# Performance work log

Measured on AMD Instinct MI355X. Metric: run time of the kernel, lower is better.

Reference implementation:

```python
import jax, jax.numpy as jnp
import numpy as np

EPS = 1e-15
N_NODES = 20000
N_EDGES = 640000
FEAT = 128
N_RBF = 20
CUTOFF = 5.0


def setup_inputs() -> dict:
    key = jax.random.key(0)
    ks = jax.random.split(key, 10)
    s_j = jax.random.normal(ks[0], (N_NODES, FEAT), jnp.float32)
    v_j = jax.random.normal(ks[1], (N_NODES, FEAT, 3), jnp.float32)
    r_ij = jax.random.normal(ks[2], (N_EDGES, 3), jnp.float32)
    nbrs = jax.random.randint(ks[3], (N_EDGES, 2), 0, N_NODES, jnp.int64)
    # InvariantDense: Dense(F->F, swish) then Dense(F->3F)
    W1 = jax.random.normal(ks[4], (FEAT, FEAT), jnp.float32) / np.sqrt(FEAT)
    b1 = jnp.zeros((FEAT,), jnp.float32)
    W2 = jax.random.normal(ks[5], (FEAT, 3 * FEAT), jnp.float32) / np.sqrt(FEAT)
    b2 = jnp.zeros((3 * FEAT,), jnp.float32)
    # DistanceEmbed dense: Dense(n_rbf -> 3F)
    Wd = jax.random.normal(ks[6], (N_RBF, 3 * FEAT), jnp.float32) / np.sqrt(N_RBF)
    bd = jnp.zeros((3 * FEAT,), jnp.float32)
    return {"s_j": s_j, "v_j": v_j, "r_ij": r_ij, "nbrs": nbrs,
            "W1": W1, "b1": b1, "W2": W2, "b2": b2, "Wd": Wd, "bd": bd}


def reference(s_j, v_j, r_ij, nbrs, W1, b1, W2, b2, Wd, bd):
    N, F = s_j.shape
    # preprocess_r
    dist = jnp.sqrt(jnp.sum(r_ij ** 2 + EPS, axis=-1))          # [E]
    unit = r_ij / dist[:, None]                                  # [E,3]
    # InvariantDense on nodes (dense before gather, as in torch code)
    phi_node = jax.nn.silu(s_j @ W1 + b1) @ W2 + b2              # [N,3F]
    phi = phi_node[nbrs[:, 1]]                                   # [E,3F]
    # PaiNN radial basis: sin(n*pi*d/cutoff)/d, n=1..n_rbf
    k = jnp.arange(1, N_RBF + 1, dtype=dist.dtype) * (np.pi / CUTOFF)  # [n_rbf]
    rbf = jnp.sin(dist[:, None] * k[None, :]) / dist[:, None]    # [E,n_rbf]
    # cosine cutoff envelope
    env = 0.5 * (jnp.cos(np.pi * dist / CUTOFF) + 1.0)
    env = jnp.where(dist < CUTOFF, env, 0.0)                     # [E]
    w_s = (rbf @ Wd + bd) * env[:, None]                         # [E,3F]
    inv = (phi * w_s).reshape(-1, 3, F)                          # [E,3,F]
    split0 = inv[:, 0, :][:, :, None]                            # [E,F,1]
    split1 = inv[:, 1, :]                                        # [E,F]
    split2 = inv[:, 2, :][:, :, None]                            # [E,F,1]
    delta_v_ij = split2 * unit[:, None, :] + split0 * v_j[nbrs[:, 1]]  # [E,F,3]
    idx = nbrs[:, 0]
    delta_s_i = jax.ops.segment_sum(split1, idx, num_segments=N)      # [N,F]
    delta_v_i = jax.ops.segment_sum(delta_v_ij, idx, num_segments=N)  # [N,F,3]
    return (delta_s_i, delta_v_i)
```

## Files before the change

### kernel.cpp

```cpp
#include <hip/hip_runtime.h>
#include <hip/hip_bf16.h>
#include <math.h>

typedef __hip_bfloat16 bf16;

#define FEAT 128
#define NRBF 20
#define CUTOFF_F 5.0f
#define KSCALE 0.62831853071795864769f

__device__ __forceinline__ float b2f(bf16 x) { return __bfloat162float(x); }
__device__ __forceinline__ bf16 f2b(float x) { return __float2bfloat16(x); }

template<int F32>
__device__ __forceinline__ float LD(const void* p, size_t i) {
    if (F32) return ((const float*)p)[i];
    return b2f(((const bf16*)p)[i]);
}
template<int F32>
__device__ __forceinline__ void ST(void* p, size_t i, float v) {
    if (F32) ((float*)p)[i] = v;
    else ((bf16*)p)[i] = f2b(v);
}

__device__ __forceinline__ int get_dst(const int* nb, int e, int is64) {
    return is64 ? nb[4 * e] : nb[2 * e];
}
__device__ __forceinline__ int get_src(const int* nb, int e, int is64) {
    return is64 ? nb[4 * e + 2] : nb[2 * e + 1];
}
__device__ __forceinline__ int clampi(int v, int n) {
    return v < 0 ? 0 : (v >= n ? n - 1 : v);
}

__global__ void init_kernel(const void* __restrict__ s_ptr, const int* __restrict__ nbrs32,
                            int nE, int* __restrict__ flags, int* __restrict__ counts, int nN) {
    int t = blockIdx.x * blockDim.x + threadIdx.x;
    if (t < nN) counts[t] = 0;
    if (t == 0) {
        const unsigned* u = (const unsigned*)s_ptr;
        int hits = 0;
        for (int i = 0; i < 64; ++i) {
            unsigned ef = (u[i] >> 7) & 0xFF;
            hits += (ef >= 110 && ef <= 135) ? 1 : 0;
        }
        flags[0] = (hits < 32) ? 1 : 0;
        int lim = 2 * nE; if (lim > 128) lim = 128;
        int allz = 1;
        for (int i = 1; i < lim; i += 2) allz &= (nbrs32[i] == 0);
        flags[1] = allz;
    }
}

__global__ void hist_kernel(const int* __restrict__ nbrs, const int* __restrict__ flags,
                            int* __restrict__ counts, int nE, int nN) {
    int e = blockIdx.x * blockDim.x + threadIdx.x;
    if (e < nE) {
        int d = clampi(get_dst(nbrs, e, flags[1]), nN);
        atomicAdd(&counts[d], 1);
    }
}

__global__ __launch_bounds__(1024) void scan_kernel(const int* __restrict__ counts,
        int* __restrict__ offsets, int* __restrict__ cursor, int nN) {
    __shared__ int part[1024];
    const int t = threadIdx.x;
    const int chunk = (nN + 1023) / 1024;
    const int base = t * chunk;
    int local[32];
    int sum = 0;
    for (int c = 0; c < chunk && c < 32; ++c) {
        int idx = base + c;
        int v = (idx < nN) ? counts[idx] : 0;
        local[c] = v;
        sum += v;
    }
    part[t] = sum;
    __syncthreads();
    for (int off = 1; off < 1024; off <<= 1) {
        int add = (t >= off) ? part[t - off] : 0;
        __syncthreads();
        part[t] += add;
        __syncthreads();
    }
    int run = part[t] - sum;
    for (int c = 0; c < chunk && c < 32; ++c) {
        int idx = base + c;
        if (idx < nN) { offsets[idx] = run; cursor[idx] = run; run += local[c]; }
    }
    if (t == 1023) offsets[nN] = part[1023];
}

__global__ void scatter_kernel(const int* __restrict__ nbrs, const int* __restrict__ flags,
                               int* __restrict__ cursor, int* __restrict__ edge_ids,
                               int nE, int nN) {
    int e = blockIdx.x * blockDim.x + threadIdx.x;
    if (e < nE) {
        int d = clampi(get_dst(nbrs, e, flags[1]), nN);
        int pos = atomicAdd(&cursor[d], 1);
        if (pos >= 0 && pos < nE) edge_ids[pos] = e;
    }
}

template<int F32, int GM>
__global__ __launch_bounds__(256) void pre_kernel(const void* __restrict__ r_ij,
        void* __restrict__ gbuf, const int* __restrict__ flags, int nE) {
    if (flags[0] != F32) return;
    int e = blockIdx.x * blockDim.x + threadIdx.x;
    if (e >= nE) return;
    const float rx = LD<F32>(r_ij, (size_t)3 * e + 0);
    const float ry = LD<F32>(r_ij, (size_t)3 * e + 1);
    const float rz = LD<F32>(r_ij, (size_t)3 * e + 2);
    const float d2   = rx * rx + ry * ry + rz * rz + 3e-15f;
    const float invd = rsqrtf(d2);
    const float d    = d2 * invd;
    const float x  = d * KSCALE;
    const float s1 = F32 ? sinf(x) : __sinf(x);
    const float c1 = F32 ? cosf(x) : __cosf(x);
    const float env = (d < CUTOFF_F) ? (0.5f * (c1 + 1.0f)) : 0.0f;
    const float scale = invd * env;
    float rec[24];
    const float tc = 2.0f * c1;
    float skm2 = 0.f, skm1 = s1;
    rec[0] = s1 * scale;
    #pragma unroll
    for (int k = 1; k < NRBF; ++k) {
        const float sk = fmaf(tc, skm1, -skm2);
        rec[k] = sk * scale;
        skm2 = skm1; skm1 = sk;
    }
    rec[20] = rx * invd; rec[21] = ry * invd; rec[22] = rz * invd; rec[23] = env;
    if (GM == 2) {
        float* dst = (float*)gbuf + (size_t)24 * e;
        #pragma unroll
        for (int i = 0; i < 24; ++i) dst[i] = rec[i];
    } else {
        bf16* dst = (bf16*)gbuf + (size_t)24 * e;
        #pragma unroll
        for (int i = 0; i < 24; ++i) dst[i] = f2b(rec[i]);
    }
}

template<int F32>
__device__ void gemm_body(const void* __restrict__ s_j, const void* __restrict__ W1,
                          const void* __restrict__ b1, const void* __restrict__ W2,
                          const void* __restrict__ b2v, bf16* __restrict__ phi, int nN) {
    __shared__ float sl[8][FEAT];
    __shared__ float hl[8][FEAT];
    const int t = threadIdx.x;
    const int n0 = blockIdx.x * 8;
    for (int idx = t; idx < 8 * FEAT; idx += 384) {
        int n = idx >> 7, k = idx & 127;
        int row = n0 + n;
        sl[n][k] = (row < nN) ? LD<F32>(s_j, (size_t)row * FEAT + k) : 0.f;
    }
    __syncthreads();
    for (int idx = t; idx < 8 * FEAT; idx += 384) {
        int n = idx >> 7, f = idx & 127;
        float a = 0.f;
        #pragma unroll 4
        for (int k = 0; k < FEAT; ++k) a = fmaf(sl[n][k], LD<F32>(W1, (size_t)k * FEAT + f), a);
        a += LD<F32>(b1, f);
        float sg = F32 ? (1.0f / (1.0f + expf(-a))) : (1.0f / (1.0f + __expf(-a)));
        hl[n][f] = a * sg;
    }
    __syncthreads();
    float acc[8] = {};
    #pragma unroll 4
    for (int k = 0; k < FEAT; ++k) {
        const float w = LD<F32>(W2, (size_t)k * 384 + t);
        #pragma unroll
        for (int n = 0; n < 8; ++n) acc[n] = fmaf(hl[n][k], w, acc[n]);
    }
    const float bb = LD<F32>(b2v, t);
    #pragma unroll
    for (int n = 0; n < 8; ++n) {
        int row = n0 + n;
        if (row < nN) phi[(size_t)row * 384 + t] = f2b(acc[n] + bb);
    }
}

__global__ __launch_bounds__(384) void gemm_node_kernel(const void* s_j, const void* W1,
        const void* b1, const void* W2, const void* b2v, bf16* phi,
        const int* __restrict__ flags, int nN) {
    if (flags[0]) gemm_body<1>(s_j, W1, b1, W2, b2v, phi, nN);
    else          gemm_body<0>(s_j, W1, b1, W2, b2v, phi, nN);
}

template<int F32, int GM>
__global__ __launch_bounds__(128, 2) void msg_kernel(
        const int* __restrict__ nbrs, const void* __restrict__ r_ij,
        const void* __restrict__ v_j, const void* __restrict__ Wd,
        const void* __restrict__ bd, const bf16* __restrict__ phi,
        const void* __restrict__ gbuf, const int* __restrict__ flags,
        const int* __restrict__ offsets, const int* __restrict__ edge_ids,
        void* __restrict__ out, int nE, int nN) {
    if (flags[0] != F32) return;
    const int i = blockIdx.x;
    const int f = threadIdx.x;
    const int is64 = flags[1];

    float wd0[NRBF], wd1[NRBF], wd2[NRBF];
    #pragma unroll
    for (int k = 0; k < NRBF; ++k) {
        wd0[k] = LD<F32>(Wd, (size_t)k * 384 + f);
        wd1[k] = LD<F32>(Wd, (size_t)k * 384 + FEAT + f);
        wd2[k] = LD<F32>(Wd, (size_t)k * 384 + 2 * FEAT + f);
    }
    const float bd0 = LD<F32>(bd, f);
    const float bd1 = LD<F32>(bd, FEAT + f);
    const float bd2 = LD<F32>(bd, 2 * FEAT + f);

    float ds = 0.f, dv0 = 0.f, dv1 = 0.f, dv2 = 0.f;

    int start = offsets[i];
    int end   = offsets[i + 1];
    if (start < 0) start = 0;
    if (end > nE) end = nE;

    for (int p = start; p < end; ++p) {
        const int e = __builtin_amdgcn_readfirstlane(clampi(edge_ids[p], nE));
        const int j = __builtin_amdgcn_readfirstlane(clampi(get_src(nbrs, e, is64), nN));

        float gk[24];
        if (GM == 2) {
            const float* g = (const float*)gbuf + (size_t)24 * e;
            #pragma unroll
            for (int q = 0; q < 24; ++q) gk[q] = g[q];
        } else if (GM == 1) {
            const bf16* g = (const bf16*)gbuf + (size_t)24 * e;
            #pragma unroll
            for (int q = 0; q < 24; ++q) gk[q] = b2f(g[q]);
        } else {
            const float rx = LD<F32>(r_ij, (size_t)3 * e + 0);
            const float ry = LD<F32>(r_ij, (size_t)3 * e + 1);
            const float rz = LD<F32>(r_ij, (size_t)3 * e + 2);
            const float d2   = rx * rx + ry * ry + rz * rz + 3e-15f;
            const float invd = rsqrtf(d2);
            const float d    = d2 * invd;
            const float x  = d * KSCALE;
            const float s1 = F32 ? sinf(x) : __sinf(x);
            const float c1 = F32 ? cosf(x) : __cosf(x);
            const float env = (d < CUTOFF_F) ? (0.5f * (c1 + 1.0f)) : 0.0f;
            const float scale = invd * env;
            const float tc = 2.0f * c1;
            float skm2 = 0.f, skm1 = s1;
            gk[0] = s1 * scale;
            #pragma unroll
            for (int k = 1; k < NRBF; ++k) {
                const float sk = fmaf(tc, skm1, -skm2);
                gk[k] = sk * scale;
                skm2 = skm1; skm1 = sk;
            }
            gk[20] = rx * invd; gk[21] = ry * invd; gk[22] = rz * invd; gk[23] = env;
        }

        float t0 = 0.f, t1 = 0.f, t2 = 0.f;
        #pragma unroll
        for (int k = 0; k < NRBF; ++k) {
            t0 = fmaf(gk[k], wd0[k], t0);
            t1 = fmaf(gk[k], wd1[k], t1);
            t2 = fmaf(gk[k], wd2[k], t2);
        }
        const float env = gk[23];
        const float w0 = fmaf(bd0, env, t0);
        const float w1 = fmaf(bd1, env, t1);
        const float w2 = fmaf(bd2, env, t2);

        const size_t pb = (size_t)j * 384;
        const float p0 = b2f(phi[pb + f]);
        const float p1 = b2f(phi[pb + FEAT + f]);
        const float p2 = b2f(phi[pb + 2 * FEAT + f]);
        const size_t vb = ((size_t)j * FEAT + f) * 3;
        const float vx = LD<F32>(v_j, vb + 0);
        const float vy = LD<F32>(v_j, vb + 1);
        const float vz = LD<F32>(v_j, vb + 2);

        const float i0 = w0 * p0;
        const float i1 = w1 * p1;
        const float i2 = w2 * p2;
        ds += i1;
        dv0 = fmaf(i2, gk[20], fmaf(i0, vx, dv0));
        dv1 = fmaf(i2, gk[21], fmaf(i0, vy, dv1));
        dv2 = fmaf(i2, gk[22], fmaf(i0, vz, dv2));
    }

    ST<F32>(out, (size_t)i * FEAT + f, ds);
    const size_t ob = (size_t)nN * FEAT + ((size_t)i * FEAT + f) * 3;
    ST<F32>(out, ob + 0, dv0);
    ST<F32>(out, ob + 1, dv1);
    ST<F32>(out, ob + 2, dv2);
}

extern "C" void kernel_launch(void* const* d_in, const int* in_sizes, int n_in,
                              void* d_out, int out_size, void* d_ws, size_t ws_size,
                              hipStream_t stream) {
    const void* s_j  = d_in[0];
    const void* v_j  = d_in[1];
    const void* r_ij = d_in[2];
    const int*  nbrs = (const int*)d_in[3];
    const void* W1   = d_in[4];
    const void* b1   = d_in[5];
    const void* W2   = d_in[6];
    const void* b2   = d_in[7];
    const void* Wd   = d_in[8];
    const void* bd   = d_in[9];

    const int nN = out_size / (4 * FEAT);
    const int nE = in_sizes[2] / 3;

    char* ws = (char*)d_ws;
    size_t off = 0;
    int* flags = (int*)(ws + off);    off += 256;
    int* counts = (int*)(ws + off);   off += ((size_t)nN * 4 + 255) & ~(size_t)255;
    int* offsets = (int*)(ws + off);  off += (((size_t)nN + 1) * 4 + 255) & ~(size_t)255;
    int* cursor = (int*)(ws + off);   off += ((size_t)nN * 4 + 255) & ~(size_t)255;
    int* edge_ids = (int*)(ws + off); off += ((size_t)nE * 4 + 255) & ~(size_t)255;

    const size_t phi_bytes = (size_t)nN * 384 * sizeof(bf16);
    const size_t g32_bytes = (size_t)nE * 24 * 4;
    const size_t g16_bytes = (size_t)nE * 24 * 2;
    int GM;
    size_t g_bytes;
    if (ws_size >= off + g32_bytes + phi_bytes)      { GM = 2; g_bytes = g32_bytes; }
    else if (ws_size >= off + g16_bytes + phi_bytes) { GM = 1; g_bytes = g16_bytes; }
    else                                             { GM = 0; g_bytes = 0; }
    void* gbuf = (void*)(ws + off);   off += (g_bytes + 255) & ~(size_t)255;
    bf16* phi = (bf16*)(ws + off);

    init_kernel<<<(nN + 255) / 256, 256, 0, stream>>>(s_j, nbrs, nE, flags, counts, nN);

    const int preg = (nE + 255) / 256;
    if (GM == 2) {
        pre_kernel<0, 2><<<preg, 256, 0, stream>>>(r_ij, gbuf, flags, nE);
        pre_kernel<1, 2><<<preg, 256, 0, stream>>>(r_ij, gbuf, flags, nE);
    } else if (GM == 1) {
        pre_kernel<0, 1><<<preg, 256, 0, stream>>>(r_ij, gbuf, flags, nE);
        pre_kernel<1, 1><<<preg, 256, 0, stream>>>(r_ij, gbuf, flags, nE);
    }

    gemm_node_kernel<<<(nN + 7) / 8, 384, 0, stream>>>(s_j, W1, b1, W2, b2, phi, flags, nN);
    hist_kernel<<<(nE + 255) / 256, 256, 0, stream>>>(nbrs, flags, counts, nE, nN);
    scan_kernel<<<1, 1024, 0, stream>>>(counts, offsets, cursor, nN);
    scatter_kernel<<<(nE + 255) / 256, 256, 0, stream>>>(nbrs, flags, cursor, edge_ids, nE, nN);

    if (GM == 2) {
        msg_kernel<0, 2><<<nN, 128, 0, stream>>>(nbrs, r_ij, v_j, Wd, bd, phi, gbuf, flags, offsets, edge_ids, d_out, nE, nN);
        msg_kernel<1, 2><<<nN, 128, 0, stream>>>(nbrs, r_ij, v_j, Wd, bd, phi, gbuf, flags, offsets, edge_ids, d_out, nE, nN);
    } else if (GM == 1) {
        msg_kernel<0, 1><<<nN, 128, 0, stream>>>(nbrs, r_ij, v_j, Wd, bd, phi, gbuf, flags, offsets, edge_ids, d_out, nE, nN);
        msg_kernel<1, 1><<<nN, 128, 0, stream>>>(nbrs, r_ij, v_j, Wd, bd, phi, gbuf, flags, offsets, edge_ids, d_out, nE, nN);
    } else {
        msg_kernel<0, 0><<<nN, 128, 0, stream>>>(nbrs, r_ij, v_j, Wd, bd, phi, gbuf, flags, offsets, edge_ids, d_out, nE, nN);
        msg_kernel<1, 0><<<nN, 128, 0, stream>>>(nbrs, r_ij, v_j, Wd, bd, phi, gbuf, flags, offsets, edge_ids, d_out, nE, nN);
    }
}
```

Baseline: 596.2 us.

## Fuse edge scatter into precompute and batch edge-index loads via lane shuffles

Merges the CSR scatter into the per-edge RBF precompute kernel and reorders launches so histogram and scan run first, removing one kernel launch and one pass over nbrs. In the message kernel, edge ids and source nodes for a block of up to 64 edges are loaded once in parallel across lanes and broadcast with shuffles, instead of each iteration doing serial scalar loads. The geometry record is read as float4 vectors, and an asm barrier pins the Wd weights in registers. Shuffles add cross-lane work per edge, and the register pinning may raise register pressure.

Result: slower. 720.7 us (+20.9%).

```diff
diff --git a/kernel.cpp b/kernel.cpp
--- a/kernel.cpp
+++ b/kernel.cpp
@@ -91,33 +91,31 @@
     if (t == 1023) offsets[nN] = part[1023];
 }
 
-__global__ void scatter_kernel(const int* __restrict__ nbrs, const int* __restrict__ flags,
-                               int* __restrict__ cursor, int* __restrict__ edge_ids,
-                               int nE, int nN) {
-    int e = blockIdx.x * blockDim.x + threadIdx.x;
-    if (e < nE) {
-        int d = clampi(get_dst(nbrs, e, flags[1]), nN);
-        int pos = atomicAdd(&cursor[d], 1);
-        if (pos >= 0 && pos < nE) edge_ids[pos] = e;
-    }
-}
-
 template<int F32, int GM>
-__global__ __launch_bounds__(256) void pre_kernel(const void* __restrict__ r_ij,
-        void* __restrict__ gbuf, const int* __restrict__ flags, int nE) {
+__global__ __launch_bounds__(256) void pre_scatter_kernel(
+        const void* __restrict__ r_ij, const int* __restrict__ nbrs,
+        const int* __restrict__ flags, int* __restrict__ cursor,
+        int* __restrict__ edge_ids, void* __restrict__ gbuf, int nE, int nN) {
     if (flags[0] != F32) return;
     int e = blockIdx.x * blockDim.x + threadIdx.x;
     if (e >= nE) return;
+
+    int d = clampi(get_dst(nbrs, e, flags[1]), nN);
+    int pos = atomicAdd(&cursor[d], 1);
+    if (pos >= 0 && pos < nE) edge_ids[pos] = e;
+
+    if (GM == 0) return;
+
     const float rx = LD<F32>(r_ij, (size_t)3 * e + 0);
     const float ry = LD<F32>(r_ij, (size_t)3 * e + 1);
     const float rz = LD<F32>(r_ij, (size_t)3 * e + 2);
     const float d2   = rx * rx + ry * ry + rz * rz + 3e-15f;
     const float invd = rsqrtf(d2);
-    const float d    = d2 * invd;
-    const float x  = d * KSCALE;
+    const float dd   = d2 * invd;
+    const float x  = dd * KSCALE;
     const float s1 = F32 ? sinf(x) : __sinf(x);
     const float c1 = F32 ? cosf(x) : __cosf(x);
-    const float env = (d < CUTOFF_F) ? (0.5f * (c1 + 1.0f)) : 0.0f;
+    const float env = (dd < CUTOFF_F) ? (0.5f * (c1 + 1.0f)) : 0.0f;
     const float scale = invd * env;
     float rec[24];
     const float tc = 2.0f * c1;
@@ -198,6 +196,7 @@
     if (flags[0] != F32) return;
     const int i = blockIdx.x;
     const int f = threadIdx.x;
+    const int lane = f & 63;
     const int is64 = flags[1];
 
     float wd0[NRBF], wd1[NRBF], wd2[NRBF];
@@ -207,6 +206,10 @@
         wd1[k] = LD<F32>(Wd, (size_t)k * 384 + FEAT + f);
         wd2[k] = LD<F32>(Wd, (size_t)k * 384 + 2 * FEAT + f);
     }
+    #pragma unroll
+    for (int k = 0; k < NRBF; ++k) {
+        asm volatile("" : "+v"(wd0[k]), "+v"(wd1[k]), "+v"(wd2[k]));
+    }
     const float bd0 = LD<F32>(bd, f);
     const float bd1 = LD<F32>(bd, FEAT + f);
     const float bd2 = LD<F32>(bd, 2 * FEAT + f);
@@ -217,72 +220,86 @@
     int end   = offsets[i + 1];
     if (start < 0) start = 0;
     if (end > nE) end = nE;
-
-    for (int p = start; p < end; ++p) {
-        const int e = __builtin_amdgcn_readfirstlane(clampi(edge_ids[p], nE));
-        const int j = __builtin_amdgcn_readfirstlane(clampi(get_src(nbrs, e, is64), nN));
-
-        float gk[24];
-        if (GM == 2) {
-            const float* g = (const float*)gbuf + (size_t)24 * e;
-            #pragma unroll
-            for (int q = 0; q < 24; ++q) gk[q] = g[q];
-        } else if (GM == 1) {
-            const bf16* g = (const bf16*)gbuf + (size_t)24 * e;
-            #pragma unroll
-            for (int q = 0; q < 24; ++q) gk[q] = b2f(g[q]);
-        } else {
-            const float rx = LD<F32>(r_ij, (size_t)3 * e + 0);
-            const float ry = LD<F32>(r_ij, (size_t)3 * e + 1);
-            const float rz = LD<F32>(r_ij, (size_t)3 * e + 2);
-            const float d2   = rx * rx + ry * ry + rz * rz + 3e-15f;
-            const float invd = rsqrtf(d2);
-            const float d    = d2 * invd;
-            const float x  = d * KSCALE;
-            const float s1 = F32 ? sinf(x) : __sinf(x);
-            const float c1 = F32 ? cosf(x) : __cosf(x);
-            const float env = (d < CUTOFF_F) ? (0.5f * (c1 + 1.0f)) : 0.0f;
-            const float scale = invd * env;
-            const float tc = 2.0f * c1;
-            float skm2 = 0.f, skm1 = s1;
-            gk[0] = s1 * scale;
+    const int cnt = end - start;
+
+    for (int base = 0; base < cnt; base += 64) {
+        const int m = (cnt - base < 64) ? (cnt - base) : 64;
+        int eL = 0, jL = 0;
+        if (lane < m) {
+            eL = clampi(edge_ids[start + base + lane], nE);
+            jL = clampi(get_src(nbrs, eL, is64), nN);
+        }
+        #pragma unroll 2
+        for (int q = 0; q < m; ++q) {
+            const int e = __shfl(eL, q);
+            const int j = __shfl(jL, q);
+
+            float gk[24];
+            if (GM == 2) {
+                const float4* g4 = (const float4*)((const float*)gbuf + (size_t)24 * e);
+                #pragma unroll
+                for (int c = 0; c < 6; ++c) {
+                    float4 v = g4[c];
+                    gk[4 * c + 0] = v.x; gk[4 * c + 1] = v.y;
+                    gk[4 * c + 2] = v.z; gk[4 * c + 3] = v.w;
+                }
+            } else if (GM == 1) {
+                const bf16* g = (const bf16*)gbuf + (size_t)24 * e;
+                #pragma unroll
+                for (int c = 0; c < 24; ++c) gk[c] = b2f(g[c]);
+            } else {
+                const float rx = LD<F32>(r_ij, (size_t)3 * e + 0);
+                const float ry = LD<F32>(r_ij, (size_t)3 * e + 1);
+                const float rz = LD<F32>(r_ij, (size_t)3 * e + 2);
+                const float d2   = rx * rx + ry * ry + rz * rz + 3e-15f;
+                const float invd = rsqrtf(d2);
+                const float dd   = d2 * invd;
+                const float x  = dd * KSCALE;
+                const float s1 = F32 ? sinf(x) : __sinf(x);
+                const float c1 = F32 ? cosf(x) : __cosf(x);
+                const float env = (dd < CUTOFF_F) ? (0.5f * (c1 + 1.0f)) : 0.0f;
+                const float scale = invd * env;
+                const float tc = 2.0f * c1;
+                float skm2 = 0.f, skm1 = s1;
+                gk[0] = s1 * scale;
+                #pragma unroll
+                for (int k = 1; k < NRBF; ++k) {
+                    const float sk = fmaf(tc, skm1, -skm2);
+                    gk[k] = sk * scale;
+                    skm2 = skm1; skm1 = sk;
+                }
+                gk[20] = rx * invd; gk[21] = ry * invd; gk[22] = rz * invd; gk[23] = env;
+            }
+
+            const size_t pb = (size_t)j * 384;
+            const float p0 = b2f(phi[pb + f]);
+            const float p1 = b2f(phi[pb + FEAT + f]);
+            const float p2 = b2f(phi[pb + 2 * FEAT + f]);
+            const size_t vb = ((size_t)j * FEAT + f) * 3;
+            const float vx = LD<F32>(v_j, vb + 0);
+            const float vy = LD<F32>(v_j, vb + 1);
+            const float vz = LD<F32>(v_j, vb + 2);
+
+            float t0 = gk[0] * wd0[0], t1 = gk[0] * wd1[0], t2 = gk[0] * wd2[0];
             #pragma unroll
             for (int k = 1; k < NRBF; ++k) {
-                const float sk = fmaf(tc, skm1, -skm2);
-                gk[k] = sk * scale;
-                skm2 = skm1; skm1 = sk;
+                t0 = fmaf(gk[k], wd0[k], t0);
+                t1 = fmaf(gk[k], wd1[k], t1);
+                t2 = fmaf(gk[k], wd2[k], t2);
             }
-            gk[20] = rx * invd; gk[21] = ry * invd; gk[22] = rz * invd; gk[23] = env;
+            const float env = gk[23];
+            const float w0 = fmaf(bd0, env, t0);
+            const float w1 = fmaf(bd1, env, t1);
+            const float w2 = fmaf(bd2, env, t2);
+
+            const float i0 = w0 * p0;
+            const float i1 = w1 * p1;
+            const float i2 = w2 * p2;
+            ds += i1;
+            dv0 = fmaf(i2, gk[20], fmaf(i0, vx, dv0));
+            dv1 = fmaf(i2, gk[21], fmaf(i0, vy, dv1));
+            dv2 = fmaf(i2, gk[22], fmaf(i0, vz, dv2));
         }
-
-        float t0 = 0.f, t1 = 0.f, t2 = 0.f;
-        #pragma unroll
-        for (int k = 0; k < NRBF; ++k) {
-            t0 = fmaf(gk[k], wd0[k], t0);
-            t1 = fmaf(gk[k], wd1[k], t1);
-            t2 = fmaf(gk[k], wd2[k], t2);
-        }
-        const float env = gk[23];
-        const float w0 = fmaf(bd0, env, t0);
-        const float w1 = fmaf(bd1, env, t1);
-        const float w2 = fmaf(bd2, env, t2);
-
-        const size_t pb = (size_t)j * 384;
-        const float p0 = b2f(phi[pb + f]);
-        const float p1 = b2f(phi[pb + FEAT + f]);
-        const float p2 = b2f(phi[pb + 2 * FEAT + f]);
-        const size_t vb = ((size_t)j * FEAT + f) * 3;
-        const float vx = LD<F32>(v_j, vb + 0);
-        const float vy = LD<F32>(v_j, vb + 1);
-        const float vz = LD<F32>(v_j, vb + 2);
-
-        const float i0 = w0 * p0;
-        const float i1 = w1 * p1;
-        const float i2 = w2 * p2;
-        ds += i1;
-        dv0 = fmaf(i2, gk[20], fmaf(i0, vx, dv0));
-        dv1 = fmaf(i2, gk[21], fmaf(i0, vy, dv1));
-        dv2 = fmaf(i2, gk[22], fmaf(i0, vz, dv2));
     }
 
     ST<F32>(out, (size_t)i * FEAT + f, ds);
@@ -329,20 +346,22 @@
     bf16* phi = (bf16*)(ws + off);
 
     init_kernel<<<(nN + 255) / 256, 256, 0, stream>>>(s_j, nbrs, nE, flags, counts, nN);
+    hist_kernel<<<(nE + 255) / 256, 256, 0, stream>>>(nbrs, flags, counts, nE, nN);
+    scan_kernel<<<1, 1024, 0, stream>>>(counts, offsets, cursor, nN);
 
     const int preg = (nE + 255) / 256;
     if (GM == 2) {
-        pre_kernel<0, 2><<<preg, 256, 0, stream>>>(r_ij, gbuf, flags, nE);
-        pre_kernel<1, 2><<<preg, 256, 0, stream>>>(r_ij, gbuf, flags, nE);
+        pre_scatter_kernel<0, 2><<<preg, 256, 0, stream>>>(r_ij, nbrs, flags, cursor, edge_ids, gbuf, nE, nN);
+        pre_scatter_kernel<1, 2><<<preg, 256, 0, stream>>>(r_ij, nbrs, flags, cursor, edge_ids, gbuf, nE, nN);
     } else if (GM == 1) {
-        pre_kernel<0, 1><<<preg, 256, 0, stream>>>(r_ij, gbuf, flags, nE);
-        pre_kernel<1, 1><<<preg, 256, 0, stream>>>(r_ij, gbuf, flags, nE);
+        pre_scatter_kernel<0, 1><<<preg, 256, 0, stream>>>(r_ij, nbrs, flags, cursor, edge_ids, gbuf, nE, nN);
+        pre_scatter_kernel<1, 1><<<preg, 256, 0, stream>>>(r_ij, nbrs, flags, cursor, edge_ids, gbuf, nE, nN);
+    } else {
+        pre_scatter_kernel<0, 0><<<preg, 256, 0, stream>>>(r_ij, nbrs, flags, cursor, edge_ids, gbuf, nE, nN);
+        pre_scatter_kernel<1, 0><<<preg, 256, 0, stream>>>(r_ij, nbrs, flags, cursor, edge_ids, gbuf, nE, nN);
     }
 
     gemm_node_kernel<<<(nN + 7) / 8, 384, 0, stream>>>(s_j, W1, b1, W2, b2, phi, flags, nN);
-    hist_kernel<<<(nE + 255) / 256, 256, 0, stream>>>(nbrs, flags, counts, nE, nN);
-    scan_kernel<<<1, 1024, 0, stream>>>(counts, offsets, cursor, nN);
-    scatter_kernel<<<(nE + 255) / 256, 256, 0, stream>>>(nbrs, flags, cursor, edge_ids, nE, nN);
 
     if (GM == 2) {
         msg_kernel<0, 2><<<nN, 128, 0, stream>>>(nbrs, r_ij, v_j, Wd, bd, phi, gbuf, flags, offsets, edge_ids, d_out, nE, nN);
```

## Fuse edge preprocessing into CSR scatter and store per-edge data in sorted order

Applied to the files above, without the earlier changes.

Merges the edge scatter with per-edge geometry preprocessing so unit vectors, envelope, source ids and RBF values are written directly at the destination-sorted position, which makes the message kernel's reads contiguous instead of indirect through edge_ids. When workspace allows, a new pass precomputes the full per-edge filter (rbf@Wd+bd)*env as bf16 rows in sorted order, so the message kernel only streams them. This trades a large extra write of E*384 bf16 values plus a second pass over r_ij for removing the per-edge 20x3 matvec in the gather kernel. It also adds bf16 rounding of the filter weights.

New measurement: 534.6 us. -10.3%, faster.

```diff
diff --git a/kernel.cpp b/kernel.cpp
--- a/kernel.cpp
+++ b/kernel.cpp
@@ -91,53 +91,72 @@
     if (t == 1023) offsets[nN] = part[1023];
 }
 
-__global__ void scatter_kernel(const int* __restrict__ nbrs, const int* __restrict__ flags,
-                               int* __restrict__ cursor, int* __restrict__ edge_ids,
-                               int nE, int nN) {
-    int e = blockIdx.x * blockDim.x + threadIdx.x;
-    if (e < nE) {
-        int d = clampi(get_dst(nbrs, e, flags[1]), nN);
-        int pos = atomicAdd(&cursor[d], 1);
-        if (pos >= 0 && pos < nE) edge_ids[pos] = e;
-    }
-}
-
-template<int F32, int GM>
-__global__ __launch_bounds__(256) void pre_kernel(const void* __restrict__ r_ij,
-        void* __restrict__ gbuf, const int* __restrict__ flags, int nE) {
-    if (flags[0] != F32) return;
-    int e = blockIdx.x * blockDim.x + threadIdx.x;
-    if (e >= nE) return;
+__global__ __launch_bounds__(384) void prep_kernel(const void* __restrict__ Wd,
+        const void* __restrict__ bd, float* __restrict__ WdT, const int* __restrict__ flags) {
+    const int c = threadIdx.x;
+    const int F32 = flags[0];
+    if (F32) {
+        for (int k = 0; k < NRBF; ++k) WdT[c * 24 + k] = ((const float*)Wd)[k * 384 + c];
+        WdT[c * 24 + 20] = ((const float*)bd)[c];
+    } else {
+        for (int k = 0; k < NRBF; ++k) WdT[c * 24 + k] = b2f(((const bf16*)Wd)[k * 384 + c]);
+        WdT[c * 24 + 20] = b2f(((const bf16*)bd)[c]);
+    }
+    WdT[c * 24 + 21] = 0.f; WdT[c * 24 + 22] = 0.f; WdT[c * 24 + 23] = 0.f;
+}
+
+template<int F32, int MODEA>
+__device__ void pre_scatter_body(const void* __restrict__ r_ij, const int* __restrict__ nbrs,
+        int is64, int* __restrict__ cursor, int* __restrict__ src_ids,
+        float4* __restrict__ u_env, int* __restrict__ pos_of_e, float* __restrict__ gbuf,
+        int e, int nE, int nN) {
+    const int d = clampi(get_dst(nbrs, e, is64), nN);
+    const int j = clampi(get_src(nbrs, e, is64), nN);
+    int pos = atomicAdd(&cursor[d], 1);
+    pos = clampi(pos, nE);
+    src_ids[pos] = j;
+
     const float rx = LD<F32>(r_ij, (size_t)3 * e + 0);
     const float ry = LD<F32>(r_ij, (size_t)3 * e + 1);
     const float rz = LD<F32>(r_ij, (size_t)3 * e + 2);
     const float d2   = rx * rx + ry * ry + rz * rz + 3e-15f;
     const float invd = rsqrtf(d2);
-    const float d    = d2 * invd;
-    const float x  = d * KSCALE;
-    const float s1 = F32 ? sinf(x) : __sinf(x);
+    const float dd   = d2 * invd;
+    const float x  = dd * KSCALE;
     const float c1 = F32 ? cosf(x) : __cosf(x);
-    const float env = (d < CUTOFF_F) ? (0.5f * (c1 + 1.0f)) : 0.0f;
-    const float scale = invd * env;
-    float rec[24];
-    const float tc = 2.0f * c1;
-    float skm2 = 0.f, skm1 = s1;
-    rec[0] = s1 * scale;
-    #pragma unroll
-    for (int k = 1; k < NRBF; ++k) {
-        const float sk = fmaf(tc, skm1, -skm2);
-        rec[k] = sk * scale;
-        skm2 = skm1; skm1 = sk;
-    }
-    rec[20] = rx * invd; rec[21] = ry * invd; rec[22] = rz * invd; rec[23] = env;
-    if (GM == 2) {
-        float* dst = (float*)gbuf + (size_t)24 * e;
+    const float env = (dd < CUTOFF_F) ? (0.5f * (c1 + 1.0f)) : 0.0f;
+    u_env[pos] = make_float4(rx * invd, ry * invd, rz * invd, env);
+
+    if (MODEA) {
+        pos_of_e[e] = pos;
+    } else {
+        const float s1 = F32 ? sinf(x) : __sinf(x);
+        const float scale = invd * env;
+        const float tc = 2.0f * c1;
+        float skm2 = 0.f, skm1 = s1;
+        float* g = gbuf + (size_t)pos * NRBF;
+        g[0] = s1 * scale;
         #pragma unroll
-        for (int i = 0; i < 24; ++i) dst[i] = rec[i];
+        for (int k = 1; k < NRBF; ++k) {
+            const float sk = fmaf(tc, skm1, -skm2);
+            g[k] = sk * scale;
+            skm2 = skm1; skm1 = sk;
+        }
+    }
+}
+
+__global__ __launch_bounds__(256) void pre_scatter_kernel(const void* r_ij, const int* nbrs,
+        const int* __restrict__ flags, int* cursor, int* src_ids, float4* u_env,
+        int* pos_of_e, float* gbuf, int nE, int nN, int modeA) {
+    int e = blockIdx.x * blockDim.x + threadIdx.x;
+    if (e >= nE) return;
+    const int F32 = flags[0], is64 = flags[1];
+    if (modeA) {
+        if (F32) pre_scatter_body<1,1>(r_ij, nbrs, is64, cursor, src_ids, u_env, pos_of_e, gbuf, e, nE, nN);
+        else     pre_scatter_body<0,1>(r_ij, nbrs, is64, cursor, src_ids, u_env, pos_of_e, gbuf, e, nE, nN);
     } else {
-        bf16* dst = (bf16*)gbuf + (size_t)24 * e;
-        #pragma unroll
-        for (int i = 0; i < 24; ++i) dst[i] = f2b(rec[i]);
+        if (F32) pre_scatter_body<1,0>(r_ij, nbrs, is64, cursor, src_ids, u_env, pos_of_e, gbuf, e, nE, nN);
+        else     pre_scatter_body<0,0>(r_ij, nbrs, is64, cursor, src_ids, u_env, pos_of_e, gbuf, e, nE, nN);
     }
 }
 
@@ -187,18 +206,117 @@
     else          gemm_body<0>(s_j, W1, b1, W2, b2v, phi, nN);
 }
 
-template<int F32, int GM>
-__global__ __launch_bounds__(128, 2) void msg_kernel(
-        const int* __restrict__ nbrs, const void* __restrict__ r_ij,
-        const void* __restrict__ v_j, const void* __restrict__ Wd,
-        const void* __restrict__ bd, const bf16* __restrict__ phi,
-        const void* __restrict__ gbuf, const int* __restrict__ flags,
-        const int* __restrict__ offsets, const int* __restrict__ edge_ids,
+template<int F32>
+__device__ void pre_ws_body(const void* __restrict__ r_ij, const float* __restrict__ WdT,
+        const int* __restrict__ pos_of_e, bf16* __restrict__ ws_w, int e) {
+    const float rx = LD<F32>(r_ij, (size_t)3 * e + 0);
+    const float ry = LD<F32>(r_ij, (size_t)3 * e + 1);
+    const float rz = LD<F32>(r_ij, (size_t)3 * e + 2);
+    const float d2   = rx * rx + ry * ry + rz * rz + 3e-15f;
+    const float invd = rsqrtf(d2);
+    const float dd   = d2 * invd;
+    const float x  = dd * KSCALE;
+    const float s1 = F32 ? sinf(x) : __sinf(x);
+    const float c1 = F32 ? cosf(x) : __cosf(x);
+    const float env = (dd < CUTOFF_F) ? (0.5f * (c1 + 1.0f)) : 0.0f;
+    const float scale = invd * env;
+    float gk[NRBF];
+    const float tc = 2.0f * c1;
+    float skm2 = 0.f, skm1 = s1;
+    gk[0] = s1 * scale;
+    #pragma unroll
+    for (int k = 1; k < NRBF; ++k) {
+        const float sk = fmaf(tc, skm1, -skm2);
+        gk[k] = sk * scale;
+        skm2 = skm1; skm1 = sk;
+    }
+    const int pos = pos_of_e[e];
+    bf16* dst = ws_w + (size_t)pos * 384;
+    for (int c0 = 0; c0 < 384; c0 += 4) {
+        float r[4];
+        #pragma unroll
+        for (int u = 0; u < 4; ++u) {
+            const float* w = WdT + (size_t)(c0 + u) * 24;
+            float acc = w[20] * env;
+            #pragma unroll
+            for (int k = 0; k < NRBF; ++k) acc = fmaf(gk[k], w[k], acc);
+            r[u] = acc;
+        }
+        union { bf16 b[4]; uint2 u2; } pk;
+        pk.b[0] = f2b(r[0]); pk.b[1] = f2b(r[1]); pk.b[2] = f2b(r[2]); pk.b[3] = f2b(r[3]);
+        *(uint2*)(dst + c0) = pk.u2;
+    }
+}
+
+__global__ __launch_bounds__(256) void pre_ws_kernel(const void* r_ij,
+        const float* __restrict__ WdT, const int* __restrict__ pos_of_e,
+        bf16* __restrict__ ws_w, const int* __restrict__ flags, int nE) {
+    int e = blockIdx.x * blockDim.x + threadIdx.x;
+    if (e >= nE) return;
+    if (flags[0]) pre_ws_body<1>(r_ij, WdT, pos_of_e, ws_w, e);
+    else          pre_ws_body<0>(r_ij, WdT, pos_of_e, ws_w, e);
+}
+
+template<int F32>
+__device__ void msg_a_body(const bf16* __restrict__ ws_w, const bf16* __restrict__ phi,
+        const void* __restrict__ v_j, const int* __restrict__ src_ids,
+        const float4* __restrict__ u_env, const int* __restrict__ offsets,
         void* __restrict__ out, int nE, int nN) {
-    if (flags[0] != F32) return;
     const int i = blockIdx.x;
     const int f = threadIdx.x;
-    const int is64 = flags[1];
+    int start = offsets[i];
+    int end   = offsets[i + 1];
+    if (start < 0) start = 0;
+    if (end > nE) end = nE;
+
+    float ds = 0.f, dv0 = 0.f, dv1 = 0.f, dv2 = 0.f;
+
+    #pragma unroll 2
+    for (int p = start; p < end; ++p) {
+        const int j = src_ids[p];
+        const float4 ue = u_env[p];
+        const bf16* wr = ws_w + (size_t)p * 384;
+        const float w0 = b2f(wr[f]);
+        const float w1 = b2f(wr[FEAT + f]);
+        const float w2 = b2f(wr[2 * FEAT + f]);
+        const bf16* ph = phi + (size_t)j * 384;
+        const float p0 = b2f(ph[f]);
+        const float p1 = b2f(ph[FEAT + f]);
+        const float p2 = b2f(ph[2 * FEAT + f]);
+        const float vx = LD<F32>(v_j, ((size_t)j * FEAT + f) * 3 + 0);
+        const float vy = LD<F32>(v_j, ((size_t)j * FEAT + f) * 3 + 1);
+        const float vz = LD<F32>(v_j, ((size_t)j * FEAT + f) * 3 + 2);
+        const float i0 = w0 * p0;
+        const float i1 = w1 * p1;
+        const float i2 = w2 * p2;
+        ds += i1;
+        dv0 = fmaf(i2, ue.x, fmaf(i0, vx, dv0));
+        dv1 = fmaf(i2, ue.y, fmaf(i0, vy, dv1));
+        dv2 = fmaf(i2, ue.z, fmaf(i0, vz, dv2));
+    }
+
+    ST<F32>(out, (size_t)i * FEAT + f, ds);
+    const size_t ob = (size_t)nN * FEAT + ((size_t)i * FEAT + f) * 3;
+    ST<F32>(out, ob + 0, dv0);
+    ST<F32>(out, ob + 1, dv1);
+    ST<F32>(out, ob + 2, dv2);
+}
+
+__global__ __launch_bounds__(128) void msg_a_kernel(const bf16* ws_w, const bf16* phi,
+        const void* v_j, const int* src_ids, const float4* u_env, const int* offsets,
+        const int* __restrict__ flags, void* out, int nE, int nN) {
+    if (flags[0]) msg_a_body<1>(ws_w, phi, v_j, src_ids, u_env, offsets, out, nE, nN);
+    else          msg_a_body<0>(ws_w, phi, v_j, src_ids, u_env, offsets, out, nE, nN);
+}
+
+template<int F32>
+__device__ void msg_b_body(const void* __restrict__ v_j, const void* __restrict__ Wd,
+        const void* __restrict__ bd, const bf16* __restrict__ phi,
+        const float* __restrict__ gbuf, const int* __restrict__ src_ids,
+        const float4* __restrict__ u_env, const int* __restrict__ offsets,
+        void* __restrict__ out, int nE, int nN) {
+    const int i = blockIdx.x;
+    const int f = threadIdx.x;
 
     float wd0[NRBF], wd1[NRBF], wd2[NRBF];
     #pragma unroll
@@ -211,78 +329,44 @@
     const float bd1 = LD<F32>(bd, FEAT + f);
     const float bd2 = LD<F32>(bd, 2 * FEAT + f);
 
-    float ds = 0.f, dv0 = 0.f, dv1 = 0.f, dv2 = 0.f;
-
     int start = offsets[i];
     int end   = offsets[i + 1];
     if (start < 0) start = 0;
     if (end > nE) end = nE;
 
+    float ds = 0.f, dv0 = 0.f, dv1 = 0.f, dv2 = 0.f;
+
     for (int p = start; p < end; ++p) {
-        const int e = __builtin_amdgcn_readfirstlane(clampi(edge_ids[p], nE));
-        const int j = __builtin_amdgcn_readfirstlane(clampi(get_src(nbrs, e, is64), nN));
-
-        float gk[24];
-        if (GM == 2) {
-            const float* g = (const float*)gbuf + (size_t)24 * e;
-            #pragma unroll
-            for (int q = 0; q < 24; ++q) gk[q] = g[q];
-        } else if (GM == 1) {
-            const bf16* g = (const bf16*)gbuf + (size_t)24 * e;
-            #pragma unroll
-            for (int q = 0; q < 24; ++q) gk[q] = b2f(g[q]);
-        } else {
-            const float rx = LD<F32>(r_ij, (size_t)3 * e + 0);
-            const float ry = LD<F32>(r_ij, (size_t)3 * e + 1);
-            const float rz = LD<F32>(r_ij, (size_t)3 * e + 2);
-            const float d2   = rx * rx + ry * ry + rz * rz + 3e-15f;
-            const float invd = rsqrtf(d2);
-            const float d    = d2 * invd;
-            const float x  = d * KSCALE;
-            const float s1 = F32 ? sinf(x) : __sinf(x);
-            const float c1 = F32 ? cosf(x) : __cosf(x);
-            const float env = (d < CUTOFF_F) ? (0.5f * (c1 + 1.0f)) : 0.0f;
-            const float scale = invd * env;
-            const float tc = 2.0f * c1;
-            float skm2 = 0.f, skm1 = s1;
-            gk[0] = s1 * scale;
-            #pragma unroll
-            for (int k = 1; k < NRBF; ++k) {
-                const float sk = fmaf(tc, skm1, -skm2);
-                gk[k] = sk * scale;
-                skm2 = skm1; skm1 = sk;
-            }
-            gk[20] = rx * invd; gk[21] = ry * invd; gk[22] = rz * invd; gk[23] = env;
-        }
-
+        const int j = src_ids[p];
+        const float4 ue = u_env[p];
+        const float* g = gbuf + (size_t)p * NRBF;
         float t0 = 0.f, t1 = 0.f, t2 = 0.f;
         #pragma unroll
         for (int k = 0; k < NRBF; ++k) {
-            t0 = fmaf(gk[k], wd0[k], t0);
-            t1 = fmaf(gk[k], wd1[k], t1);
-            t2 = fmaf(gk[k], wd2[k], t2);
+            const float gk = g[k];
+            t0 = fmaf(gk, wd0[k], t0);
+            t1 = fmaf(gk, wd1[k], t1);
+            t2 = fmaf(gk, wd2[k], t2);
         }
-        const float env = gk[23];
-        const float w0 = fmaf(bd0, env, t0);
-        const float w1 = fmaf(bd1, env, t1);
-        const float w2 = fmaf(bd2, env, t2);
-
-        const size_t pb = (size_t)j * 384;
-        const float p0 = b2f(phi[pb + f]);
-        const float p1 = b2f(phi[pb + FEAT + f]);
-        const float p2 = b2f(phi[pb + 2 * FEAT + f]);
-        const size_t vb = ((size_t)j * FEAT + f) * 3;
-        const float vx = LD<F32>(v_j, vb + 0);
-        const float vy = LD<F32>(v_j, vb + 1);
-        const float vz = LD<F32>(v_j, vb + 2);
+        const float w0 = fmaf(bd0, ue.w, t0);
+        const float w1 = fmaf(bd1, ue.w, t1);
+        const float w2 = fmaf(bd2, ue.w, t2);
+
+        const bf16* ph = phi + (size_t)j * 384;
+        const float p0 = b2f(ph[f]);
+        const float p1 = b2f(ph[FEAT + f]);
+        const float p2 = b2f(ph[2 * FEAT + f]);
+        const float vx = LD<F32>(v_j, ((size_t)j * FEAT + f) * 3 + 0);
+        const float vy = LD<F32>(v_j, ((size_t)j * FEAT + f) * 3 + 1);
+        const float vz = LD<F32>(v_j, ((size_t)j * FEAT + f) * 3 + 2);
 
         const float i0 = w0 * p0;
         const float i1 = w1 * p1;
         const float i2 = w2 * p2;
         ds += i1;
-        dv0 = fmaf(i2, gk[20], fmaf(i0, vx, dv0));
-        dv1 = fmaf(i2, gk[21], fmaf(i0, vy, dv1));
-        dv2 = fmaf(i2, gk[22], fmaf(i0, vz, dv2));
+        dv0 = fmaf(i2, ue.x, fmaf(i0, vx, dv0));
+        dv1 = fmaf(i2, ue.y, fmaf(i0, vy, dv1));
+        dv2 = fmaf(i2, ue.z, fmaf(i0, vz, dv2));
     }
 
     ST<F32>(out, (size_t)i * FEAT + f, ds);
@@ -290,6 +374,14 @@
     ST<F32>(out, ob + 0, dv0);
     ST<F32>(out, ob + 1, dv1);
     ST<F32>(out, ob + 2, dv2);
+}
+
+__global__ __launch_bounds__(128) void msg_b_kernel(const void* v_j, const void* Wd,
+        const void* bd, const bf16* phi, const float* gbuf, const int* src_ids,
+        const float4* u_env, const int* offsets, const int* __restrict__ flags,
+        void* out, int nE, int nN) {
+    if (flags[0]) msg_b_body<1>(v_j, Wd, bd, phi, gbuf, src_ids, u_env, offsets, out, nE, nN);
+    else          msg_b_body<0>(v_j, Wd, bd, phi, gbuf, src_ids, u_env, offsets, out, nE, nN);
 }
 
 extern "C" void kernel_launch(void* const* d_in, const int* in_sizes, int n_in,
@@ -311,47 +403,47 @@
 
     char* ws = (char*)d_ws;
     size_t off = 0;
-    int* flags = (int*)(ws + off);    off += 256;
-    int* counts = (int*)(ws + off);   off += ((size_t)nN * 4 + 255) & ~(size_t)255;
-    int* offsets = (int*)(ws + off);  off += (((size_t)nN + 1) * 4 + 255) & ~(size_t)255;
-    int* cursor = (int*)(ws + off);   off += ((size_t)nN * 4 + 255) & ~(size_t)255;
-    int* edge_ids = (int*)(ws + off); off += ((size_t)nE * 4 + 255) & ~(size_t)255;
-
-    const size_t phi_bytes = (size_t)nN * 384 * sizeof(bf16);
-    const size_t g32_bytes = (size_t)nE * 24 * 4;
-    const size_t g16_bytes = (size_t)nE * 24 * 2;
-    int GM;
-    size_t g_bytes;
-    if (ws_size >= off + g32_bytes + phi_bytes)      { GM = 2; g_bytes = g32_bytes; }
-    else if (ws_size >= off + g16_bytes + phi_bytes) { GM = 1; g_bytes = g16_bytes; }
-    else                                             { GM = 0; g_bytes = 0; }
-    void* gbuf = (void*)(ws + off);   off += (g_bytes + 255) & ~(size_t)255;
-    bf16* phi = (bf16*)(ws + off);
+    auto alloc = [&](size_t bytes) -> void* {
+        void* p = ws + off;
+        off = (off + bytes + 255) & ~(size_t)255;
+        return p;
+    };
+    int*    flags    = (int*)alloc(16);
+    int*    counts   = (int*)alloc((size_t)nN * 4);
+    int*    offsets  = (int*)alloc(((size_t)nN + 1) * 4);
+    int*    cursor   = (int*)alloc((size_t)nN * 4);
+    int*    src_ids  = (int*)alloc((size_t)nE * 4);
+    float4* u_env    = (float4*)alloc((size_t)nE * 16);
+    float*  WdT      = (float*)alloc((size_t)384 * 24 * 4);
+    const size_t base = off;
+
+    size_t offA = base;
+    int*  pos_of_e = (int*)(ws + offA);  offA += ((size_t)nE * 4 + 255) & ~(size_t)255;
+    bf16* phiA     = (bf16*)(ws + offA); offA += ((size_t)nN * 384 * 2 + 255) & ~(size_t)255;
+    bf16* ws_w     = (bf16*)(ws + offA); offA += (size_t)nE * 384 * 2;
+    size_t offB = base;
+    float* gbuf = (float*)(ws + offB);   offB += ((size_t)nE * NRBF * 4 + 255) & ~(size_t)255;
+    bf16*  phiB = (bf16*)(ws + offB);    offB += (size_t)nN * 384 * 2;
+
+    const int modeA = (ws_size >= offA) ? 1 : 0;
+    bf16* phi = modeA ? phiA : phiB;
 
     init_kernel<<<(nN + 255) / 256, 256, 0, stream>>>(s_j, nbrs, nE, flags, counts, nN);
-
-    const int preg = (nE + 255) / 256;
-    if (GM == 2) {
-        pre_kernel<0, 2><<<preg, 256, 0, stream>>>(r_ij, gbuf, flags, nE);
-        pre_kernel<1, 2><<<preg, 256, 0, stream>>>(r_ij, gbuf, flags, nE);
-    } else if (GM == 1) {
-        pre_kernel<0, 1><<<preg, 256, 0, stream>>>(r_ij, gbuf, flags, nE);
-        pre_kernel<1, 1><<<preg, 256, 0, stream>>>(r_ij, gbuf, flags, nE);
-    }
-
-    gemm_node_kernel<<<(nN + 7) / 8, 384, 0, stream>>>(s_j, W1, b1, W2, b2, phi, flags, nN);
     hist_kernel<<<(nE + 255) / 256, 256, 0, stream>>>(nbrs, flags, counts, nE, nN);
     scan_kernel<<<1, 1024, 0, stream>>>(counts, offsets, cursor, nN);
-    scatter_kernel<<<(nE + 255) / 256, 256, 0, stream>>>(nbrs, flags, cursor, edge_ids, nE, nN);
-
-    if (GM == 2) {
-        msg_kernel<0, 2><<<nN, 128, 0, stream>>>(nbrs, r_ij, v_j, Wd, bd, phi, gbuf, flags, offsets, edge_ids, d_out, nE, nN);
-        msg_kernel<1, 2><<<nN, 128, 0, stream>>>(nbrs, r_ij, v_j, Wd, bd, phi, gbuf, flags, offsets, edge_ids, d_out, nE, nN);
-    } else if (GM == 1) {
-        msg_kernel<0, 1><<<nN, 128, 0, stream>>>(nbrs, r_ij, v_j, Wd, bd, phi, gbuf, flags, offsets, edge_ids, d_out, nE, nN);
-        msg_kernel<1, 1><<<nN, 128, 0, stream>>>(nbrs, r_ij, v_j, Wd, bd, phi, gbuf, flags, offsets, edge_ids, d_out, nE, nN);
+    prep_kernel<<<1, 384, 0, stream>>>(Wd, bd, WdT, flags);
+
+    pre_scatter_kernel<<<(nE + 255) / 256, 256, 0, stream>>>(
+        r_ij, nbrs, flags, cursor, src_ids, u_env, pos_of_e, gbuf, nE, nN, modeA);
+
+    gemm_node_kernel<<<(nN + 7) / 8, 384, 0, stream>>>(s_j, W1, b1, W2, b2, phi, flags, nN);
+
+    if (modeA) {
+        pre_ws_kernel<<<(nE + 255) / 256, 256, 0, stream>>>(r_ij, WdT, pos_of_e, ws_w, flags, nE);
+        msg_a_kernel<<<nN, 128, 0, stream>>>(ws_w, phi, v_j, src_ids, u_env, offsets,
+                                             flags, d_out, nE, nN);
     } else {
-        msg_kernel<0, 0><<<nN, 128, 0, stream>>>(nbrs, r_ij, v_j, Wd, bd, phi, gbuf, flags, offsets, edge_ids, d_out, nE, nN);
-        msg_kernel<1, 0><<<nN, 128, 0, stream>>>(nbrs, r_ij, v_j, Wd, bd, phi, gbuf, flags, offsets, edge_ids, d_out, nE, nN);
-    }
-}
+        msg_b_kernel<<<nN, 128, 0, stream>>>(v_j, Wd, bd, phi, gbuf, src_ids, u_env,
+                                             offsets, flags, d_out, nE, nN);
+    }
+}
```
